# Optimization experiments

Measured on AMD Instinct MI355X. Metric: run time of the kernel, lower is better.

Reference implementation:

```python
import jax, jax.numpy as jnp
import numpy as np

N_NODES, N_GRAPHS, PER_GRAPH, N_EDGES = 20000, 200, 100, 320000
X_DIM, E_DIM, G_DIM = 32, 16, 32
NUM_EMB, HEADS, LAYERS = 64, 2, 3
EPS_GEN, EPS_LN = 1e-7, 1e-5


def _w(k, shape, scale=0.05):
    return (jax.random.normal(k, shape) * scale).astype(jnp.float32)


def _mlp3(x, W1, b1, W2, b2, W3, b3):
    h = jax.nn.leaky_relu(x @ W1 + b1)
    h = jax.nn.leaky_relu(h @ W2 + b2)
    return h @ W3 + b3


def _seg_sum(x, idx, n):
    return jax.ops.segment_sum(x, idx, num_segments=n)


def _seg_mean(x, idx, n):
    s = _seg_sum(x, idx, n)
    cnt = _seg_sum(jnp.ones((x.shape[0],), x.dtype), idx, n)
    return s / jnp.clip(cnt, 1.0, None)[:, None]


def _seg_softmax(logits, idx, n):
    # PyG softmax: subtract per-segment max, normalize with +1e-16
    m = jax.ops.segment_max(logits, idx, num_segments=n)
    m = jnp.where(jnp.isfinite(m), m, 0.0)
    e = jnp.exp(logits - m[idx])
    s = jax.ops.segment_sum(e, idx, num_segments=n)
    return e / (s[idx] + 1e-16)


def _graph_layernorm(x, batch, n_graphs):
    # PyG LayerNorm(mode='graph', affine=False): mean/var over all node-feature
    # entries of each graph.
    f = x.shape[-1]
    cnt = _seg_sum(jnp.ones((x.shape[0],), x.dtype), batch, n_graphs)
    norm = jnp.clip(cnt, 1.0, None) * f
    mean = _seg_sum(x.sum(-1), batch, n_graphs) / norm
    xc = x - mean[batch][:, None]
    var = _seg_sum((xc * xc).sum(-1), batch, n_graphs) / norm
    return xc / jnp.sqrt(var + EPS_LN)[batch][:, None]


def _forward(x, edge_attr, cond, edge_index, batch,
             x2h_W1, x2h_b1, x2h_W2, x2h_b2, x2h_W3, x2h_b3,
             e2h_W1, e2h_b1, e2h_W2, e2h_b2, e2h_W3, e2h_b3,
             c2h_W1, c2h_b1, c2h_W2, c2h_b2, c2h_W3, c2h_b3,
             gen_W, tr_Wq, tr_bq, tr_Wk, tr_bk, tr_Wv, tr_bv, tr_We, tr_Ws, tr_bs,
             lin_W, lin_b, ff_W1, ff_b1, ff_W2, ff_b2):
    N = x.shape[0]
    G = cond.shape[0]
    Naug = N + G
    o = _mlp3(x, x2h_W1, x2h_b1, x2h_W2, x2h_b2, x2h_W3, x2h_b3)
    e = _mlp3(edge_attr, e2h_W1, e2h_b1, e2h_W2, e2h_b2, e2h_W3, e2h_b3)
    c = _mlp3(cond, c2h_W1, c2h_b1, c2h_W2, c2h_b2, c2h_W3, c2h_b3)
    # virtual-node edges: node<->virtual node of its graph (virtual ids = N..N+G-1)
    u = jnp.arange(N, dtype=edge_index.dtype)
    v = batch.astype(edge_index.dtype) + N
    aug_ei = jnp.concatenate([edge_index, jnp.stack([u, v]), jnp.stack([v, u])], axis=1)
    e_p = jnp.zeros((2 * N, NUM_EMB), o.dtype).at[:, 0].set(1.0)
    aug_e = jnp.concatenate([e, e_p], axis=0)
    # add_self_loops(fill_value='mean'): self-loop attr = mean of incoming edge attrs
    loop_attr = _seg_mean(aug_e, aug_ei[1], Naug)
    loops = jnp.arange(Naug, dtype=edge_index.dtype)
    aug_ei = jnp.concatenate([aug_ei, jnp.stack([loops, loops])], axis=1)
    aug_e = jnp.concatenate([aug_e, loop_attr], axis=0)
    aug_batch = jnp.concatenate([batch, jnp.arange(G, dtype=batch.dtype)])
    o = jnp.concatenate([o, c], axis=0)  # [Naug, emb]
    src, dst = aug_ei[0], aug_ei[1]
    scale = 1.0 / float(np.sqrt(NUM_EMB))
    for i in range(LAYERS):
        # GENConv(aggr='add', norm=None, num_layers=1): sum(relu(x_j+e)+eps) + x, then Linear
        msg = jax.nn.relu(o[src] + aug_e) + EPS_GEN
        agg = (_seg_sum(msg, dst, Naug) + o) @ gen_W[i]
        # TransformerConv(2*emb -> emb, heads, edge_dim=emb, concat=True)
        xin = jnp.concatenate([o, agg], axis=1)  # [Naug, 2*emb]
        q = (xin @ tr_Wq[i] + tr_bq[i]).reshape(Naug, HEADS, NUM_EMB)
        k = (xin @ tr_Wk[i] + tr_bk[i]).reshape(Naug, HEADS, NUM_EMB)
        vv = (xin @ tr_Wv[i] + tr_bv[i]).reshape(Naug, HEADS, NUM_EMB)
        eh = (aug_e @ tr_We[i]).reshape(-1, HEADS, NUM_EMB)  # [E, H, C]
        kj = k[src] + eh
        alpha = _seg_softmax(jnp.einsum('ehc,ehc->eh', q[dst], kj) * scale, dst, Naug)
        tout = _seg_sum((vv[src] + eh) * alpha[..., None], dst, Naug)
        tout = tout.reshape(Naug, HEADS * NUM_EMB) + xin @ tr_Ws[i] + tr_bs[i]
        # residual + graph LayerNorm, then FFN + graph LayerNorm
        o = _graph_layernorm(o + tout @ lin_W[i] + lin_b[i], aug_batch, G)
        ff = jax.nn.leaky_relu(o @ ff_W1[i] + ff_b1[i]) @ ff_W2[i] + ff_b2[i]
        o = _graph_layernorm(o + ff, aug_batch, G)
    node_o, virt = o[:N], o[N:]
    glob = jnp.concatenate([_seg_mean(node_o, batch, G), virt, c], axis=1)
    o_final = jnp.concatenate([node_o, c[batch]], axis=1)
    return (o_final, glob)


def setup_inputs() -> dict:
    key = jax.random.key(0)
    ks = iter(jax.random.split(key, 64))
    inp = {}
    inp['x'] = jax.random.normal(next(ks), (N_NODES, X_DIM), dtype=jnp.float32)
    inp['edge_attr'] = jax.random.normal(next(ks), (N_EDGES, E_DIM), dtype=jnp.float32)
    inp['cond'] = jax.random.normal(next(ks), (N_GRAPHS, G_DIM), dtype=jnp.float32)
    src = jax.random.randint(next(ks), (N_EDGES,), 0, N_NODES)
    dst = (src // PER_GRAPH) * PER_GRAPH + jax.random.randint(next(ks), (N_EDGES,), 0, PER_GRAPH)
    inp['edge_index'] = jnp.stack([src, dst]).astype(jnp.int32)
    inp['batch'] = jnp.repeat(jnp.arange(N_GRAPHS, dtype=jnp.int32), PER_GRAPH)
    for p, nin in [('x2h', X_DIM), ('e2h', E_DIM), ('c2h', G_DIM)]:
        inp[p + '_W1'] = _w(next(ks), (nin, NUM_EMB)); inp[p + '_b1'] = _w(next(ks), (NUM_EMB,))
        inp[p + '_W2'] = _w(next(ks), (NUM_EMB, NUM_EMB)); inp[p + '_b2'] = _w(next(ks), (NUM_EMB,))
        inp[p + '_W3'] = _w(next(ks), (NUM_EMB, NUM_EMB)); inp[p + '_b3'] = _w(next(ks), (NUM_EMB,))
    HC = HEADS * NUM_EMB
    inp['gen_W'] = _w(next(ks), (LAYERS, NUM_EMB, NUM_EMB))
    inp['tr_Wq'] = _w(next(ks), (LAYERS, 2 * NUM_EMB, HC)); inp['tr_bq'] = _w(next(ks), (LAYERS, HC))
    inp['tr_Wk'] = _w(next(ks), (LAYERS, 2 * NUM_EMB, HC)); inp['tr_bk'] = _w(next(ks), (LAYERS, HC))
    inp['tr_Wv'] = _w(next(ks), (LAYERS, 2 * NUM_EMB, HC)); inp['tr_bv'] = _w(next(ks), (LAYERS, HC))
    inp['tr_We'] = _w(next(ks), (LAYERS, NUM_EMB, HC))
    inp['tr_Ws'] = _w(next(ks), (LAYERS, 2 * NUM_EMB, HC)); inp['tr_bs'] = _w(next(ks), (LAYERS, HC))
    inp['lin_W'] = _w(next(ks), (LAYERS, HC, NUM_EMB)); inp['lin_b'] = _w(next(ks), (LAYERS, NUM_EMB))
    inp['ff_W1'] = _w(next(ks), (LAYERS, NUM_EMB, 4 * NUM_EMB)); inp['ff_b1'] = _w(next(ks), (LAYERS, 4 * NUM_EMB))
    inp['ff_W2'] = _w(next(ks), (LAYERS, 4 * NUM_EMB, NUM_EMB)); inp['ff_b2'] = _w(next(ks), (LAYERS, NUM_EMB))
    return inp


def reference(x, edge_attr, cond, edge_index, batch,
              x2h_W1, x2h_b1, x2h_W2, x2h_b2, x2h_W3, x2h_b3,
              e2h_W1, e2h_b1, e2h_W2, e2h_b2, e2h_W3, e2h_b3,
              c2h_W1, c2h_b1, c2h_W2, c2h_b2, c2h_W3, c2h_b3,
              gen_W, tr_Wq, tr_bq, tr_Wk, tr_bk, tr_Wv, tr_bv, tr_We, tr_Ws, tr_bs,
              lin_W, lin_b, ff_W1, ff_b1, ff_W2, ff_b2):
    return _forward(x, edge_attr, cond, edge_index, batch,
                    x2h_W1, x2h_b1, x2h_W2, x2h_b2, x2h_W3, x2h_b3,
                    e2h_W1, e2h_b1, e2h_W2, e2h_b2, e2h_W3, e2h_b3,
                    c2h_W1, c2h_b1, c2h_W2, c2h_b2, c2h_W3, c2h_b3,
                    gen_W, tr_Wq, tr_bq, tr_Wk, tr_bk, tr_Wv, tr_bv, tr_We, tr_Ws, tr_bs,
                    lin_W, lin_b, ff_W1, ff_b1, ff_W2, ff_b2)
```

## Files before the change

### kernel.cpp

```cpp
#include <hip/hip_runtime.h>
#include <cstddef>

#define NN   20000
#define NG   200
#define NE   320000
#define NAUG 20200
#define NE2  360000
#define EAUG 380200
#define DD   64
#define HC   128

typedef float  f32x4 __attribute__((ext_vector_type(4)));
typedef short  s16x8 __attribute__((ext_vector_type(8)));

static __device__ __forceinline__ unsigned short bf16r(float f){
  unsigned u = __float_as_uint(f);
  u += 0x7FFFu + ((u >> 16) & 1u);
  return (unsigned short)(u >> 16);
}
static __device__ __forceinline__ float4 b2f4(ushort4 u){
  return make_float4(__uint_as_float((unsigned)u.x << 16),
                     __uint_as_float((unsigned)u.y << 16),
                     __uint_as_float((unsigned)u.z << 16),
                     __uint_as_float((unsigned)u.w << 16));
}
static __device__ __forceinline__ float d4(float4 a, float4 b){
  return a.x*b.x + a.y*b.y + a.z*b.z + a.w*b.w;
}
static __device__ __forceinline__ float4 f4ab(float4 a, float s, float4 b, float t){
  return make_float4(a.x*s + b.x*t, a.y*s + b.y*t, a.z*s + b.z*t, a.w*s + b.w*t);
}
static __device__ __forceinline__ float4 f4s(float4 a, float s){
  return make_float4(a.x*s, a.y*s, a.z*s, a.w*s);
}

#define WTAB_INIT { \
  {0,0,128,128,136,128,0},{0,0,128,128,136,128,16384},{0,0,128,128,136,128,32768}, \
  {1,0,128,128,136,128,0},{1,0,128,128,136,128,16384},{1,0,128,128,136,128,32768}, \
  {2,0,128,128,136,128,0},{2,0,128,128,136,128,16384},{2,0,128,128,136,128,32768}, \
  {3,0,128,128,136,128,0},{3,0,128,128,136,128,16384},{3,0,128,128,136,128,32768}, \
  {4,0,64,64,72,64,0},{4,0,64,64,72,64,4096},{4,0,64,64,72,64,8192}, \
  {5,0,128,64,136,64,0},{5,0,128,64,136,64,8192},{5,0,128,64,136,64,16384}, \
  {6,0,64,256,72,256,0},{6,0,64,256,72,256,16384},{6,0,64,256,72,256,32768}, \
  {7,0,256,64,264,64,0},{7,0,256,64,264,64,16384},{7,0,256,64,264,64,32768}, \
  {8,1,64,64,72,128,0},{8,1,64,64,72,128,64},{8,1,64,64,72,128,8192},{8,1,64,64,72,128,8256},{8,1,64,64,72,128,16384},{8,1,64,64,72,128,16448}, \
  {8,0,64,64,72,128,0},{8,0,64,64,72,128,64},{8,0,64,64,72,128,8192},{8,0,64,64,72,128,8256},{8,0,64,64,72,128,16384},{8,0,64,64,72,128,16448}, \
  {9,0,32,64,40,64,0},{10,0,64,64,72,64,0},{11,0,64,64,72,64,0}, \
  {12,0,16,64,40,64,0},{13,0,64,64,72,64,0},{14,0,64,64,72,64,0}, \
  {15,0,32,64,40,64,0},{16,0,64,64,72,64,0},{17,0,64,64,72,64,0} }

static const int WTAB_H[45][7] = WTAB_INIT;
__device__ static const int WTAB_D[45][7] = WTAB_INIT;

struct WPtrs { const float* p[18]; };

__global__ void wconv_all_k(WPtrs wp, unsigned short* __restrict__ outbase){
  int b = blockIdx.x;
  int acc = 0; unsigned ooff = 0;
  #pragma unroll 1
  for (int j = 0; j < 45; j++){
    int e  = WTAB_D[j][3] * WTAB_D[j][4];
    int nb = (e + 255) >> 8;
    if (b < acc + nb){
      int idx = (b - acc)*256 + threadIdx.x;
      if (idx < e){
        int KP = WTAB_D[j][4];
        int n = idx / KP, k = idx % KP;
        float v = 0.f;
        if (k < WTAB_D[j][2]){
          const float* s = wp.p[WTAB_D[j][0]];
          int st = WTAB_D[j][5], so = WTAB_D[j][6];
          v = (WTAB_D[j][1] == 0) ? s[(size_t)so + (size_t)k*st + n]
                                  : s[(size_t)so + (size_t)n*st + k];
        }
        outbase[ooff + idx] = bf16r(v);
      }
      return;
    }
    acc += nb; ooff += (unsigned)e;
  }
}

template<int NT>
__launch_bounds__(256)
__global__ void gemm_mfma_k(const float* __restrict__ A, const float* __restrict__ A2,
                            int M, int K, int lda,
                            const unsigned short* __restrict__ WtG,
                            const float* __restrict__ bias, int act,
                            const float* __restrict__ res, const float* __restrict__ res2,
                            int rstride, float* __restrict__ out, int ostride){
  extern __shared__ unsigned short smem[];
  const int KC  = (K > 128) ? 128 : K;
  const int KPc = KC + 8;
  const int KP  = K + 8;
  unsigned short* Wts  = smem;
  unsigned short* Asub = smem + NT*KPc;
  const int tid = threadIdx.x;
  const int wid = tid >> 6, lane = tid & 63;
  const int lrow = lane & 15, quad = lane >> 4;
  const int m0 = blockIdx.x * 64;
  f32x4 acc[NT/16];
  #pragma unroll
  for (int t = 0; t < NT/16; t++) acc[t] = (f32x4){0.f,0.f,0.f,0.f};

  for (int k0 = 0; k0 < K; k0 += KC){
    const int wv = NT*KPc/8, wrow = KPc/8;
    for (int i = tid; i < wv; i += 256){
      int n = i / wrow, c8 = i % wrow;
      *(uint4*)&Wts[n*KPc + c8*8] = *(const uint4*)&WtG[(size_t)n*KP + k0 + c8*8];
    }
    const int av = 64*KC/4, arow = KC/4;
    for (int i = tid; i < av; i += 256){
      int r = i / arow, c4i = i % arow;
      int m = m0 + r, k = k0 + c4i*4;
      float4 v = make_float4(0.f,0.f,0.f,0.f);
      if (m < M){
        v = *(const float4*)(A + (size_t)m*lda + k);
        if (A2){ float4 w = *(const float4*)(A2 + (size_t)m*lda + k);
                 v.x += w.x; v.y += w.y; v.z += w.z; v.w += w.w; }
      }
      ushort4 s; s.x = bf16r(v.x); s.y = bf16r(v.y); s.z = bf16r(v.z); s.w = bf16r(v.w);
      *(ushort4*)&Asub[r*KPc + c4i*4] = s;
    }
    __syncthreads();
    const int ksteps = KC >> 5;
    for (int ks = 0; ks < ksteps; ks++){
      s16x8 a = *(const s16x8*)&Asub[(wid*16 + lrow)*KPc + ks*32 + quad*8];
      #pragma unroll
      for (int nt = 0; nt < NT/16; nt++){
        s16x8 b = *(const s16x8*)&Wts[(nt*16 + lrow)*KPc + ks*32 + quad*8];
        acc[nt] = __builtin_amdgcn_mfma_f32_16x16x32_bf16(a, b, acc[nt], 0, 0, 0);
      }
    }
    __syncthreads();
  }

  const int mb = m0 + wid*16 + quad*4;
  #pragma unroll
  for (int nt = 0; nt < NT/16; nt++){
    int n = nt*16 + lrow;
    #pragma unroll
    for (int r = 0; r < 4; r++){
      int m = mb + r;
      if (m < M){
        float v = acc[nt][r];
        if (bias) v += bias[n];
        if (act)  v = v > 0.f ? v : 0.01f*v;
        if (res)  v += res [(size_t)m*rstride + n];
        if (res2) v += res2[(size_t)m*rstride + n];
        out[(size_t)m*ostride + n] = v;
      }
    }
  }
}

struct PW4 { const unsigned short* w[4]; const float* b[4]; };

__launch_bounds__(256)
__global__ void qkvs4_k(const float* __restrict__ A, int M, PW4 pw,
                        float* __restrict__ out){
  __shared__ __align__(16) unsigned short Wts[128*136];
  __shared__ __align__(16) unsigned short Asub[64*136];
  const unsigned short* WtG = pw.w[blockIdx.y];
  const float* bias = pw.b[blockIdx.y];
  const int tid = threadIdx.x;
  const int wid = tid >> 6, lane = tid & 63;
  const int lrow = lane & 15, quad = lane >> 4;
  const int m0 = blockIdx.x * 64;
  for (int i = tid; i < 128*17; i += 256){
    int n = i/17, c8 = i%17;
    *(uint4*)&Wts[n*136 + c8*8] = *(const uint4*)&WtG[(size_t)n*136 + c8*8];
  }
  for (int i = tid; i < 64*32; i += 256){
    int r = i >> 5, c4 = (i & 31)*4;
    int m = m0 + r;
    float4 v = make_float4(0.f,0.f,0.f,0.f);
    if (m < M) v = *(const float4*)(A + (size_t)m*128 + c4);
    ushort4 s; s.x=bf16r(v.x); s.y=bf16r(v.y); s.z=bf16r(v.z); s.w=bf16r(v.w);
    *(ushort4*)&Asub[r*136 + c4] = s;
  }
  __syncthreads();
  f32x4 acc[8];
  #pragma unroll
  for (int t=0;t<8;t++) acc[t] = (f32x4){0.f,0.f,0.f,0.f};
  #pragma unroll
  for (int ks = 0; ks < 4; ks++){
    s16x8 a = *(const s16x8*)&Asub[(wid*16 + lrow)*136 + ks*32 + quad*8];
    #pragma unroll
    for (int nt = 0; nt < 8; nt++){
      s16x8 b = *(const s16x8*)&Wts[(nt*16 + lrow)*136 + ks*32 + quad*8];
      acc[nt] = __builtin_amdgcn_mfma_f32_16x16x32_bf16(a, b, acc[nt], 0, 0, 0);
    }
  }
  const int mb = m0 + wid*16 + quad*4;
  const int yoff = blockIdx.y*128;
  #pragma unroll
  for (int nt = 0; nt < 8; nt++){
    int n = nt*16 + lrow;
    #pragma unroll
    for (int r = 0; r < 4; r++){
      int m = mb + r;
      if (m < M) out[(size_t)m*512 + yoff + n] = acc[nt][r] + bias[n];
    }
  }
}

struct PW2 { const unsigned short* w[2]; };

__launch_bounds__(256)
__global__ void qe2_k(const float* __restrict__ qkvs, int M, PW2 pw,
                      float* __restrict__ qe){
  __shared__ __align__(16) unsigned short Wts[64*72];
  __shared__ __align__(16) unsigned short Asub[64*72];
  const unsigned short* WtG = pw.w[blockIdx.y];
  const int tid = threadIdx.x;
  const int wid = tid >> 6, lane = tid & 63;
  const int lrow = lane & 15, quad = lane >> 4;
  const int m0 = blockIdx.x * 64;
  const int yoff = blockIdx.y * 64;
  for (int i = tid; i < 64*9; i += 256){
    int n = i/9, c8 = i%9;
    *(uint4*)&Wts[n*72 + c8*8] = *(const uint4*)&WtG[(size_t)n*72 + c8*8];
  }
  for (int i = tid; i < 64*16; i += 256){
    int r = i >> 4, c4 = (i & 15)*4;
    int m = m0 + r;
    float4 v = make_float4(0.f,0.f,0.f,0.f);
    if (m < M) v = *(const float4*)(qkvs + (size_t)m*512 + yoff + c4);
    ushort4 s; s.x=bf16r(v.x); s.y=bf16r(v.y); s.z=bf16r(v.z); s.w=bf16r(v.w);
    *(ushort4*)&Asub[r*72 + c4] = s;
  }
  __syncthreads();
  f32x4 acc[4];
  #pragma unroll
  for (int t=0;t<4;t++) acc[t] = (f32x4){0.f,0.f,0.f,0.f};
  #pragma unroll
  for (int ks = 0; ks < 2; ks++){
    s16x8 a = *(const s16x8*)&Asub[(wid*16 + lrow)*72 + ks*32 + quad*8];
    #pragma unroll
    for (int nt = 0; nt < 4; nt++){
      s16x8 b = *(const s16x8*)&Wts[(nt*16 + lrow)*72 + ks*32 + quad*8];
      acc[nt] = __builtin_amdgcn_mfma_f32_16x16x32_bf16(a, b, acc[nt], 0, 0, 0);
    }
  }
  const int mb = m0 + wid*16 + quad*4;
  #pragma unroll
  for (int nt = 0; nt < 4; nt++){
    int n = nt*16 + lrow;
    #pragma unroll
    for (int r = 0; r < 4; r++){
      int m = mb + r;
      if (m < M) qe[(size_t)m*HC + yoff + n] = acc[nt][r];
    }
  }
}

__launch_bounds__(256)
__global__ void tout2_k(const float* __restrict__ wv, int M, PW2 pw,
                        const float* __restrict__ t1, const float* __restrict__ qkvs,
                        float* __restrict__ tout){
  __shared__ __align__(16) unsigned short Wts[64*72];
  __shared__ __align__(16) unsigned short Asub[64*72];
  const unsigned short* WtG = pw.w[blockIdx.y];
  const int tid = threadIdx.x;
  const int wid = tid >> 6, lane = tid & 63;
  const int lrow = lane & 15, quad = lane >> 4;
  const int m0 = blockIdx.x * 64;
  const int yoff = blockIdx.y * 64;
  for (int i = tid; i < 64*9; i += 256){
    int n = i/9, c8 = i%9;
    *(uint4*)&Wts[n*72 + c8*8] = *(const uint4*)&WtG[(size_t)n*72 + c8*8];
  }
  for (int i = tid; i < 64*16; i += 256){
    int r = i >> 4, c4 = (i & 15)*4;
    int m = m0 + r;
    float4 v = make_float4(0.f,0.f,0.f,0.f);
    if (m < M) v = *(const float4*)(wv + (size_t)m*HC + yoff + c4);
    ushort4 s; s.x=bf16r(v.x); s.y=bf16r(v.y); s.z=bf16r(v.z); s.w=bf16r(v.w);
    *(ushort4*)&Asub[r*72 + c4] = s;
  }
  __syncthreads();
  f32x4 acc[4];
  #pragma unroll
  for (int t=0;t<4;t++) acc[t] = (f32x4){0.f,0.f,0.f,0.f};
  #pragma unroll
  for (int ks = 0; ks < 2; ks++){
    s16x8 a = *(const s16x8*)&Asub[(wid*16 + lrow)*72 + ks*32 + quad*8];
    #pragma unroll
    for (int nt = 0; nt < 4; nt++){
      s16x8 b = *(const s16x8*)&Wts[(nt*16 + lrow)*72 + ks*32 + quad*8];
      acc[nt] = __builtin_amdgcn_mfma_f32_16x16x32_bf16(a, b, acc[nt], 0, 0, 0);
    }
  }
  const int mb = m0 + wid*16 + quad*4;
  #pragma unroll
  for (int nt = 0; nt < 4; nt++){
    int n = nt*16 + lrow;
    #pragma unroll
    for (int r = 0; r < 4; r++){
      int m = mb + r;
      if (m < M)
        tout[(size_t)m*HC + yoff + n] = acc[nt][r]
          + t1[(size_t)m*HC + yoff + n] + qkvs[(size_t)m*512 + 384 + yoff + n];
    }
  }
}

__launch_bounds__(256)
__global__ void mlp3_mfma_k(const float* __restrict__ X, int M, int Din,
                            const unsigned short* __restrict__ w1t,
                            const unsigned short* __restrict__ w2t,
                            const unsigned short* __restrict__ w3t,
                            const float* __restrict__ b1, const float* __restrict__ b2,
                            const float* __restrict__ b3, float* __restrict__ out){
  __shared__ __align__(16) unsigned short W1s[64*40], W2s[64*72], W3s[64*72];
  __shared__ __align__(16) unsigned short xs[64*40], hs[64*72];
  __shared__ float bsh[192];
  const int tid = threadIdx.x;
  for (int i = tid; i < 320; i += 256)  *(uint4*)&W1s[i*8] = *(const uint4*)&w1t[i*8];
  for (int i = tid; i < 576; i += 256){ *(uint4*)&W2s[i*8] = *(const uint4*)&w2t[i*8];
                                        *(uint4*)&W3s[i*8] = *(const uint4*)&w3t[i*8]; }
  if (tid < 64){ bsh[tid] = b1[tid]; bsh[64+tid] = b2[tid]; bsh[128+tid] = b3[tid]; }
  const int m0 = blockIdx.x * 64;
  for (int i = tid; i < 512; i += 256){
    int r = i >> 3, c4 = (i & 7) * 4;
    int m = m0 + r;
    float4 v = make_float4(0.f,0.f,0.f,0.f);
    if (m < M && c4 < Din) v = *(const float4*)(X + (size_t)m*Din + c4);
    ushort4 s; s.x = bf16r(v.x); s.y = bf16r(v.y); s.z = bf16r(v.z); s.w = bf16r(v.w);
    *(ushort4*)&xs[r*40 + c4] = s;
  }
  __syncthreads();
  const int wid = tid >> 6, lane = tid & 63;
  const int lrow = lane & 15, quad = lane >> 4;
  f32x4 acc[4];

  #pragma unroll
  for (int t = 0; t < 4; t++) acc[t] = (f32x4){0.f,0.f,0.f,0.f};
  {
    s16x8 a = *(const s16x8*)&xs[(wid*16 + lrow)*40 + quad*8];
    #pragma unroll
    for (int nt = 0; nt < 4; nt++){
      s16x8 b = *(const s16x8*)&W1s[(nt*16 + lrow)*40 + quad*8];
      acc[nt] = __builtin_amdgcn_mfma_f32_16x16x32_bf16(a, b, acc[nt], 0, 0, 0);
    }
  }
  #pragma unroll
  for (int nt = 0; nt < 4; nt++){
    int n = nt*16 + lrow;
    #pragma unroll
    for (int r = 0; r < 4; r++){
      float v = acc[nt][r] + bsh[n];
      v = v > 0.f ? v : 0.01f*v;
      hs[(wid*16 + quad*4 + r)*72 + n] = bf16r(v);
    }
  }
  __syncthreads();

  #pragma unroll
  for (int t = 0; t < 4; t++) acc[t] = (f32x4){0.f,0.f,0.f,0.f};
  #pragma unroll
  for (int ks = 0; ks < 2; ks++){
    s16x8 a = *(const s16x8*)&hs[(wid*16 + lrow)*72 + ks*32 + quad*8];
    #pragma unroll
    for (int nt = 0; nt < 4; nt++){
      s16x8 b = *(const s16x8*)&W2s[(nt*16 + lrow)*72 + ks*32 + quad*8];
      acc[nt] = __builtin_amdgcn_mfma_f32_16x16x32_bf16(a, b, acc[nt], 0, 0, 0);
    }
  }
  __syncthreads();
  #pragma unroll
  for (int nt = 0; nt < 4; nt++){
    int n = nt*16 + lrow;
    #pragma unroll
    for (int r = 0; r < 4; r++){
      float v = acc[nt][r] + bsh[64 + n];
      v = v > 0.f ? v : 0.01f*v;
      hs[(wid*16 + quad*4 + r)*72 + n] = bf16r(v);
    }
  }
  __syncthreads();

  #pragma unroll
  for (int t = 0; t < 4; t++) acc[t] = (f32x4){0.f,0.f,0.f,0.f};
  #pragma unroll
  for (int ks = 0; ks < 2; ks++){
    s16x8 a = *(const s16x8*)&hs[(wid*16 + lrow)*72 + ks*32 + quad*8];
    #pragma unroll
    for (int nt = 0; nt < 4; nt++){
      s16x8 b = *(const s16x8*)&W3s[(nt*16 + lrow)*72 + ks*32 + quad*8];
      acc[nt] = __builtin_amdgcn_mfma_f32_16x16x32_bf16(a, b, acc[nt], 0, 0, 0);
    }
  }
  #pragma unroll
  for (int nt = 0; nt < 4; nt++){
    int n = nt*16 + lrow;
    #pragma unroll
    for (int r = 0; r < 4; r++){
      int m = m0 + wid*16 + quad*4 + r;
      if (m < M) out[(size_t)m*64 + n] = acc[nt][r] + bsh[128 + n];
    }
  }
}

__global__ void build_edges_k(const int* __restrict__ ei, const int* __restrict__ batch,
                              int* __restrict__ srcA, int* __restrict__ dstA){
  int idx = blockIdx.x*256 + threadIdx.x;
  if (idx >= EAUG) return;
  int s, d;
  if (idx < NE)          { s = ei[idx];              d = ei[NE+idx]; }
  else if (idx < NE+NN)  { int i = idx-NE;           s = i;            d = batch[i]+NN; }
  else if (idx < NE2)    { int i = idx-(NE+NN);      s = batch[i]+NN;  d = i; }
  else                   { int i = idx-NE2;          s = i;            d = i; }
  srcA[idx]=s; dstA[idx]=d;
}

__global__ void count_k(const int* __restrict__ dstA, int* __restrict__ cnt){
  int e = blockIdx.x*256 + threadIdx.x;
  if (e < EAUG) atomicAdd(&cnt[dstA[e]], 1);
}

__global__ void scan_k(const int* __restrict__ cnt, int* __restrict__ rowptr){
  __shared__ int part[1024];
  int tid = threadIdx.x;
  const int per = (NAUG + 1023) / 1024;
  int base = tid * per;
  int s = 0;
  for (int i=0;i<per;i++){ int idx=base+i; if (idx<NAUG) s += cnt[idx]; }
  part[tid] = s;
  __syncthreads();
  for (int off=1; off<1024; off<<=1){
    int v = (tid>=off) ? part[tid-off] : 0;
    __syncthreads();
    part[tid] += v;
    __syncthreads();
  }
  int run = (tid==0) ? 0 : part[tid-1];
  for (int i=0;i<per;i++){
    int idx=base+i;
    if (idx<NAUG){ rowptr[idx]=run; run += cnt[idx]; }
  }
  if (tid==0) rowptr[NAUG] = EAUG;
}

__global__ void scatter_k(const int* __restrict__ srcA, const int* __restrict__ dstA,
                          const int* __restrict__ rowptr, int* __restrict__ cursor,
                          int* __restrict__ eid, int* __restrict__ esrc){
  int e = blockIdx.x*256 + threadIdx.x;
  if (e >= EAUG) return;
  int d = dstA[e];
  int pos = rowptr[d] + atomicAdd(&cursor[d], 1);
  eid[pos]  = e;
  esrc[pos] = srcA[e];
}

__global__ void set_ep_k(float* __restrict__ aug_e){
  int idx = blockIdx.x*256 + threadIdx.x;
  if (idx >= 2*NN*DD) return;
  int c = idx & 63;
  aug_e[(size_t)NE*DD + idx] = (c==0) ? 1.f : 0.f;
}

__launch_bounds__(256)
__global__ void loopmean_k(const int* __restrict__ rowptr, const int* __restrict__ eid,
                           float* __restrict__ aug_e){
  int tid = threadIdx.x;
  int d = blockIdx.x*16 + (tid>>4);
  if (d >= NAUG) return;
  int t4 = (tid & 15)*4;
  int beg = rowptr[d], end = rowptr[d+1];
  float4 s = make_float4(0.f,0.f,0.f,0.f); int n = 0;
  for (int p=beg; p<end; p++){
    int e = eid[p];
    if (e < NE2){
      float4 a = *(const float4*)(aug_e + (size_t)e*DD + t4);
      s.x += a.x; s.y += a.y; s.z += a.z; s.w += a.w;
      n++;
    }
  }
  float cv = (n < 1) ? 1.f : (float)n;
  *(float4*)(aug_e + (size_t)(NE2+d)*DD + t4) = f4s(s, 1.f/cv);
}

__launch_bounds__(512)
__global__ void msg_graph_k(const float* __restrict__ o, const float* __restrict__ aug_e,
                            const int* __restrict__ rowptr, const int* __restrict__ eid,
                            const int* __restrict__ esrc, float* __restrict__ aggsum){
  __shared__ __align__(16) float OS[101*72];
  const int g = blockIdx.x;
  const int tid = threadIdx.x;
  for (int i = tid; i < 101*16; i += 512){
    int ln = i >> 4, c4 = (i & 15)*4;
    int row = (ln < 100) ? g*100 + ln : NN + g;
    *(float4*)&OS[ln*72 + c4] = *(const float4*)(o + (size_t)row*DD + c4);
  }
  __syncthreads();
  const int gr = tid >> 4;
  const int t4 = (tid & 15)*4;
  for (int ld = gr; ld < 101; ld += 32){
    int d = (ld < 100) ? g*100 + ld : NN + g;
    int beg = rowptr[d], end = rowptr[d+1];
    float4 acc = make_float4(0.f,0.f,0.f,0.f);
    for (int p=beg; p<end; p++){
      int e = eid[p], s = esrc[p];
      int ls = (s >= NN) ? 100 : (s - g*100);
      float4 ov = *(const float4*)&OS[ls*72 + t4];
      float4 ae = *(const float4*)(aug_e + (size_t)e*DD + t4);
      acc.x += fmaxf(ov.x+ae.x, 0.f) + 1e-7f;
      acc.y += fmaxf(ov.y+ae.y, 0.f) + 1e-7f;
      acc.z += fmaxf(ov.z+ae.z, 0.f) + 1e-7f;
      acc.w += fmaxf(ov.w+ae.w, 0.f) + 1e-7f;
    }
    *(float4*)(aggsum + (size_t)d*DD + t4) = acc;
  }
}

__global__ void copy_o_xin_k(const float* __restrict__ o, float* __restrict__ xin){
  int idx = blockIdx.x*256 + threadIdx.x;
  if (idx >= NAUG*DD) return;
  int n = idx >> 6, c = idx & 63;
  xin[(size_t)n*HC + c] = o[idx];
}

__launch_bounds__(512)
__global__ void attn_graph_k(const float* __restrict__ qkvs, const float* __restrict__ qe,
                             const float* __restrict__ aug_e,
                             const int* __restrict__ rowptr, const int* __restrict__ eid,
                             const int* __restrict__ esrc,
                             float* __restrict__ t1, float* __restrict__ wbuf){
  __shared__ __align__(16) unsigned short KV[101*264];
  const int g = blockIdx.x;
  const int tid = threadIdx.x;
  for (int i = tid; i < 101*64; i += 512){
    int ln = i >> 6, c4 = (i & 63)*4;
    int row = (ln < 100) ? g*100 + ln : NN + g;
    float4 v = *(const float4*)(qkvs + (size_t)row*512 + 128 + c4);
    ushort4 s; s.x=bf16r(v.x); s.y=bf16r(v.y); s.z=bf16r(v.z); s.w=bf16r(v.w);
    *(ushort4*)&KV[ln*264 + c4] = s;
  }
  __syncthreads();
  const int gr = tid >> 4;
  const int t4 = (tid & 15)*4;
  for (int ld = gr; ld < 101; ld += 32){
    int d = (ld < 100) ? g*100 + ld : NN + g;
    const float* qr = qkvs + (size_t)d*512;
    float4 q0  = *(const float4*)(qr + t4);
    float4 q1  = *(const float4*)(qr + 64 + t4);
    float4 qe0 = *(const float4*)(qe + (size_t)d*HC + t4);
    float4 qe1 = *(const float4*)(qe + (size_t)d*HC + 64 + t4);
    float m0=-1e30f, m1=-1e30f, l0=0.f, l1=0.f;
    float4 a0 = make_float4(0.f,0.f,0.f,0.f), a1 = a0, w0 = a0, w1 = a0;
    int beg = rowptr[d], end = rowptr[d+1];
    for (int p=beg; p<end; p++){
      int e = eid[p], s = esrc[p];
      int ls = (s >= NN) ? 100 : (s - g*100);
      const unsigned short* kr = &KV[ls*264];
      float4 k0 = b2f4(*(const ushort4*)(kr + t4));
      float4 k1 = b2f4(*(const ushort4*)(kr + 64 + t4));
      float4 v0 = b2f4(*(const ushort4*)(kr + 128 + t4));
      float4 v1 = b2f4(*(const ushort4*)(kr + 192 + t4));
      float4 ae = *(const float4*)(aug_e + (size_t)e*DD + t4);
      float p0 = d4(q0,k0) + d4(qe0,ae);
      float p1 = d4(q1,k1) + d4(qe1,ae);
      p0 += __shfl_xor(p0,8); p0 += __shfl_xor(p0,4); p0 += __shfl_xor(p0,2); p0 += __shfl_xor(p0,1);
      p1 += __shfl_xor(p1,8); p1 += __shfl_xor(p1,4); p1 += __shfl_xor(p1,2); p1 += __shfl_xor(p1,1);
      p0 *= 0.125f; p1 *= 0.125f;
      float nm0 = fmaxf(m0, p0);
      float sc0 = __expf(m0 - nm0);
      float e0  = __expf(p0 - nm0);
      l0 = l0*sc0 + e0; a0 = f4ab(a0, sc0, v0, e0); w0 = f4ab(w0, sc0, ae, e0); m0 = nm0;
      float nm1 = fmaxf(m1, p1);
      float sc1 = __expf(m1 - nm1);
      float e1  = __expf(p1 - nm1);
      l1 = l1*sc1 + e1; a1 = f4ab(a1, sc1, v1, e1); w1 = f4ab(w1, sc1, ae, e1); m1 = nm1;
    }
    float i0 = 1.f/(l0 + 1e-16f), i1 = 1.f/(l1 + 1e-16f);
    *(float4*)(t1   + (size_t)d*HC + t4)      = f4s(a0, i0);
    *(float4*)(t1   + (size_t)d*HC + 64 + t4) = f4s(a1, i1);
    *(float4*)(wbuf + (size_t)d*HC + t4)      = f4s(w0, i0);
    *(float4*)(wbuf + (size_t)d*HC + 64 + t4) = f4s(w1, i1);
  }
}

__global__ void ln_k(const float* __restrict__ y, float* __restrict__ o){
  int g = blockIdx.x, tid = threadIdx.x;
  float sum=0.f, ss=0.f;
  for (int i=tid; i<101*64; i+=256){
    int nd=i>>6, c=i&63;
    int row = (nd<100) ? g*100+nd : NN+g;
    float v = y[(size_t)row*DD + c];
    sum += v; ss += v*v;
  }
  #pragma unroll
  for (int off=32; off; off>>=1){ sum += __shfl_xor(sum, off); ss += __shfl_xor(ss, off); }
  __shared__ float s1[4], s2[4];
  if ((tid&63)==0){ s1[tid>>6]=sum; s2[tid>>6]=ss; }
  __syncthreads();
  sum = s1[0]+s1[1]+s1[2]+s1[3];
  ss  = s2[0]+s2[1]+s2[2]+s2[3];
  const float inv = 1.f/6464.f;
  float mean = sum*inv;
  float var  = ss*inv - mean*mean;
  float rstd = rsqrtf(var + 1e-5f);
  for (int i=tid; i<101*64; i+=256){
    int nd=i>>6, c=i&63;
    int row = (nd<100) ? g*100+nd : NN+g;
    o[(size_t)row*DD + c] = (y[(size_t)row*DD + c] - mean)*rstd;
  }
}

__global__ void copy_c_o_k(const float* __restrict__ c_emb, float* __restrict__ o){
  int idx = blockIdx.x*256 + threadIdx.x;
  if (idx >= NG*DD) return;
  o[(size_t)NN*DD + idx] = c_emb[idx];
}

__global__ void glob_k(const float* __restrict__ o, const float* __restrict__ c_emb,
                       float* __restrict__ gout){
  int g = blockIdx.x, c = threadIdx.x;
  float acc = 0.f;
  for (int t=0;t<100;t++) acc += o[(size_t)(g*100+t)*DD + c];
  gout[(size_t)g*192 + c]       = acc / 100.f;
  gout[(size_t)g*192 + 64 + c]  = o[(size_t)(NN+g)*DD + c];
  gout[(size_t)g*192 + 128 + c] = c_emb[(size_t)g*DD + c];
}
__global__ void ofinal_k(const float* __restrict__ o, const float* __restrict__ c_emb,
                         const int* __restrict__ batch, float* __restrict__ out){
  int idx = blockIdx.x*256 + threadIdx.x;
  if (idx >= NN*HC) return;
  int n = idx>>7, j = idx&127;
  out[idx] = (j<64) ? o[(size_t)n*DD + j] : c_emb[(size_t)batch[n]*DD + (j-64)];
}

static inline int cdiv(int a, int b){ return (a+b-1)/b; }

static inline void gemm_mfma(int N, const float* A, const float* A2, int M, int K, int lda,
                             const unsigned short* Wt, const float* bias, int act,
                             const float* res, const float* res2, int rstride,
                             float* out, int ostride, hipStream_t st){
  int KC = (K > 128) ? 128 : K;
  int KPc = KC + 8;
  size_t sh = (size_t)(N*KPc + 64*KPc) * 2;
  int grid = cdiv(M, 64);
  if (N == 64)
    gemm_mfma_k<64><<<grid,256,sh,st>>>(A,A2,M,K,lda,Wt,bias,act,res,res2,rstride,out,ostride);
  else if (N == 128)
    gemm_mfma_k<128><<<grid,256,sh,st>>>(A,A2,M,K,lda,Wt,bias,act,res,res2,rstride,out,ostride);
  else
    gemm_mfma_k<256><<<grid,256,sh,st>>>(A,A2,M,K,lda,Wt,bias,act,res,res2,rstride,out,ostride);
}

extern "C" void kernel_launch(void* const* d_in, const int* in_sizes, int n_in,
                              void* d_out, int out_size, void* d_ws, size_t ws_size,
                              hipStream_t stream){
  (void)in_sizes; (void)n_in; (void)out_size;
  const float* x         = (const float*)d_in[0];
  const float* edge_attr = (const float*)d_in[1];
  const float* cond      = (const float*)d_in[2];
  const int*   edge_index= (const int*)  d_in[3];
  const int*   batch     = (const int*)  d_in[4];
  const float* xW1=(const float*)d_in[5],  *xb1=(const float*)d_in[6],
             * xW2=(const float*)d_in[7],  *xb2=(const float*)d_in[8],
             * xW3=(const float*)d_in[9],  *xb3=(const float*)d_in[10];
  const float* eW1=(const float*)d_in[11], *eb1=(const float*)d_in[12],
             * eW2=(const float*)d_in[13], *eb2=(const float*)d_in[14],
             * eW3=(const float*)d_in[15], *eb3=(const float*)d_in[16];
  const float* cW1=(const float*)d_in[17], *cb1=(const float*)d_in[18],
             * cW2=(const float*)d_in[19], *cb2=(const float*)d_in[20],
             * cW3=(const float*)d_in[21], *cb3=(const float*)d_in[22];
  const float* gen_W=(const float*)d_in[23];
  const float* trWq=(const float*)d_in[24], *trbq=(const float*)d_in[25];
  const float* trWk=(const float*)d_in[26], *trbk=(const float*)d_in[27];
  const float* trWv=(const float*)d_in[28], *trbv=(const float*)d_in[29];
  const float* trWe=(const float*)d_in[30];
  const float* trWs=(const float*)d_in[31], *trbs=(const float*)d_in[32];
  const float* linW=(const float*)d_in[33], *linb=(const float*)d_in[34];
  const float* ffW1=(const float*)d_in[35], *ffb1=(const float*)d_in[36];
  const float* ffW2=(const float*)d_in[37], *ffb2=(const float*)d_in[38];
  float* out = (float*)d_out;

  float* ws = (float*)d_ws;
  size_t off = 0;
  auto alloc = [&](size_t n)->float*{ float* p = ws + off; off += (n + 63) & ~(size_t)63; return p; };
  int*      srcA  = (int*)alloc(EAUG);
  int*      dstA  = (int*)alloc(EAUG);
  int*      cnt   = (int*)alloc(NAUG);
  int*      rowptr= (int*)alloc(NAUG+1);
  int*      cursor= (int*)alloc(NAUG);
  int*      eid   = (int*)alloc(EAUG);
  int*      esrc  = (int*)alloc(EAUG);
  float*    aug_e = alloc((size_t)EAUG*DD);
  float*    o     = alloc((size_t)NAUG*DD);
  float*    c_emb = alloc((size_t)NG*DD);
  float*    ybuf  = alloc((size_t)NAUG*DD);
  float*    aggsum= alloc((size_t)NAUG*DD);
  float*    xin   = alloc((size_t)NAUG*HC);
  float*    xqkvs = alloc((size_t)NAUG*512);
  float*    qeb   = alloc((size_t)NAUG*HC);
  float*    toutb = alloc((size_t)NAUG*HC);
  float*    t1    = alloc((size_t)NAUG*HC);
  float*    wbuf  = alloc((size_t)NAUG*HC);
  float*    ffh   = alloc((size_t)NAUG*256);
  unsigned short* warena = (unsigned short*)alloc(222720);
  if (off*sizeof(float) > ws_size) return;

  const unsigned short* wptr[45];
  int wblk = 0;
  { size_t woff = 0;
    for (int j = 0; j < 45; j++){
      wptr[j] = warena + woff;
      int e = WTAB_H[j][3]*WTAB_H[j][4];
      woff += (size_t)e;
      wblk += cdiv(e, 256);
    } }

  WPtrs wp;
  wp.p[0]=trWq; wp.p[1]=trWk; wp.p[2]=trWv; wp.p[3]=trWs; wp.p[4]=gen_W;
  wp.p[5]=linW; wp.p[6]=ffW1; wp.p[7]=ffW2; wp.p[8]=trWe;
  wp.p[9]=xW1; wp.p[10]=xW2; wp.p[11]=xW3;
  wp.p[12]=eW1; wp.p[13]=eW2; wp.p[14]=eW3;
  wp.p[15]=cW1; wp.p[16]=cW2; wp.p[17]=cW3;
  wconv_all_k<<<wblk,256,0,stream>>>(wp, warena);

  build_edges_k<<<cdiv(EAUG,256),256,0,stream>>>(edge_index, batch, srcA, dstA);
  hipMemsetAsync(cnt, 0, sizeof(int)*NAUG, stream);
  hipMemsetAsync(cursor, 0, sizeof(int)*NAUG, stream);
  count_k<<<cdiv(EAUG,256),256,0,stream>>>(dstA, cnt);
  scan_k<<<1,1024,0,stream>>>(cnt, rowptr);
  scatter_k<<<cdiv(EAUG,256),256,0,stream>>>(srcA, dstA, rowptr, cursor, eid, esrc);

  mlp3_mfma_k<<<cdiv(NN,64),256,0,stream>>>(x,        NN, 32, wptr[36],wptr[37],wptr[38], xb1,xb2,xb3, o);
  mlp3_mfma_k<<<cdiv(NG,64),256,0,stream>>>(cond,     NG, 32, wptr[42],wptr[43],wptr[44], cb1,cb2,cb3, c_emb);
  mlp3_mfma_k<<<cdiv(NE,64),256,0,stream>>>(edge_attr,NE, 16, wptr[39],wptr[40],wptr[41], eb1,eb2,eb3, aug_e);
  set_ep_k<<<cdiv(2*NN*DD,256),256,0,stream>>>(aug_e);
  loopmean_k<<<cdiv(NAUG,16),256,0,stream>>>(rowptr, eid, aug_e);
  copy_c_o_k<<<cdiv(NG*DD,256),256,0,stream>>>(c_emb, o);

  for (int L=0; L<3; L++){
    const float* lb_i = linb + (size_t)L*DD;
    const float* f1b  = ffb1 + (size_t)L*256;
    const float* f2b  = ffb2 + (size_t)L*DD;
    const unsigned short* genT = wptr[12+L], *linT = wptr[15+L], *ff1T = wptr[18+L], *ff2T = wptr[21+L];
    PW4 pw4; pw4.w[0]=wptr[0+L]; pw4.w[1]=wptr[3+L]; pw4.w[2]=wptr[6+L]; pw4.w[3]=wptr[9+L];
    pw4.b[0]=trbq+(size_t)L*HC; pw4.b[1]=trbk+(size_t)L*HC;
    pw4.b[2]=trbv+(size_t)L*HC; pw4.b[3]=trbs+(size_t)L*HC;
    PW2 pwE; pwE.w[0]=wptr[24+2*L]; pwE.w[1]=wptr[25+2*L];
    PW2 pwT; pwT.w[0]=wptr[30+2*L]; pwT.w[1]=wptr[31+2*L];

    msg_graph_k<<<NG,512,0,stream>>>(o, aug_e, rowptr, eid, esrc, aggsum);
    copy_o_xin_k<<<cdiv(NAUG*DD,256),256,0,stream>>>(o, xin);
    gemm_mfma( 64, aggsum, o, NAUG, 64, 64, genT, nullptr, 0, nullptr, nullptr, 0, xin+64, HC, stream);
    qkvs4_k<<<dim3(cdiv(NAUG,64),4),256,0,stream>>>(xin, NAUG, pw4, xqkvs);
    qe2_k<<<dim3(cdiv(NAUG,64),2),256,0,stream>>>(xqkvs, NAUG, pwE, qeb);
    attn_graph_k<<<NG,512,0,stream>>>(xqkvs, qeb, aug_e, rowptr, eid, esrc, t1, wbuf);
    tout2_k<<<dim3(cdiv(NAUG,64),2),256,0,stream>>>(wbuf, NAUG, pwT, t1, xqkvs, toutb);
    gemm_mfma( 64, toutb, nullptr, NAUG, 128, 128, linT, lb_i, 0, o, nullptr, DD, ybuf, DD, stream);
    ln_k<<<NG,256,0,stream>>>(ybuf, o);
    gemm_mfma(256, o,   nullptr, NAUG,  64,  64, ff1T, f1b, 1, nullptr, nullptr, 0, ffh, 256, stream);
    gemm_mfma( 64, ffh, nullptr, NAUG, 256, 256, ff2T, f2b, 0, o, nullptr, DD, ybuf, DD, stream);
    ln_k<<<NG,256,0,stream>>>(ybuf, o);
  }

  glob_k<<<NG,64,0,stream>>>(o, c_emb, out + (size_t)NN*HC);
  ofinal_k<<<cdiv(NN*HC,256),256,0,stream>>>(o, c_emb, batch, out);
}
```

Before: 1.466 ms.

## Store edge embeddings in CSR order and split per-graph kernels across two blocks

Edge features are now written directly in destination-sorted CSR order using a per-edge position map, so the message and attention kernels read them contiguously by CSR position instead of gathering through eid. Per-graph source indices are preloaded into shared memory as bytes. The msg and attn kernels launch two blocks per graph, each handling half of the destination nodes, to raise occupancy. In exchange the edge MLP and init kernels now do scattered writes, and the node embeddings are loaded into shared memory twice per graph.

```diff
diff --git a/kernel.cpp b/kernel.cpp
--- a/kernel.cpp
+++ b/kernel.cpp
@@ -312,7 +312,8 @@
                             const unsigned short* __restrict__ w2t,
                             const unsigned short* __restrict__ w3t,
                             const float* __restrict__ b1, const float* __restrict__ b2,
-                            const float* __restrict__ b3, float* __restrict__ out){
+                            const float* __restrict__ b3,
+                            const int* __restrict__ perm, float* __restrict__ out){
   __shared__ __align__(16) unsigned short W1s[64*40], W2s[64*72], W3s[64*72];
   __shared__ __align__(16) unsigned short xs[64*40], hs[64*72];
   __shared__ float bsh[192];
@@ -398,7 +399,10 @@
     #pragma unroll
     for (int r = 0; r < 4; r++){
       int m = m0 + wid*16 + quad*4 + r;
-      if (m < M) out[(size_t)m*64 + n] = acc[nt][r] + bsh[128 + n];
+      if (m < M){
+        int orow = perm ? perm[m] : m;
+        out[(size_t)orow*64 + n] = acc[nt][r] + bsh[128 + n];
+      }
     }
   }
 }
@@ -445,25 +449,27 @@
 
 __global__ void scatter_k(const int* __restrict__ srcA, const int* __restrict__ dstA,
                           const int* __restrict__ rowptr, int* __restrict__ cursor,
-                          int* __restrict__ eid, int* __restrict__ esrc){
+                          int* __restrict__ eid, int* __restrict__ esrc,
+                          int* __restrict__ epos){
   int e = blockIdx.x*256 + threadIdx.x;
   if (e >= EAUG) return;
   int d = dstA[e];
   int pos = rowptr[d] + atomicAdd(&cursor[d], 1);
   eid[pos]  = e;
   esrc[pos] = srcA[e];
-}
-
-__global__ void set_ep_k(float* __restrict__ aug_e){
+  epos[e]   = pos;
+}
+
+__global__ void set_ep_k(const int* __restrict__ epos, float* __restrict__ aug_p){
   int idx = blockIdx.x*256 + threadIdx.x;
   if (idx >= 2*NN*DD) return;
-  int c = idx & 63;
-  aug_e[(size_t)NE*DD + idx] = (c==0) ? 1.f : 0.f;
+  int i = idx >> 6, c = idx & 63;
+  aug_p[(size_t)epos[NE + i]*DD + c] = (c==0) ? 1.f : 0.f;
 }
 
 __launch_bounds__(256)
 __global__ void loopmean_k(const int* __restrict__ rowptr, const int* __restrict__ eid,
-                           float* __restrict__ aug_e){
+                           const int* __restrict__ epos, float* __restrict__ aug_p){
   int tid = threadIdx.x;
   int d = blockIdx.x*16 + (tid>>4);
   if (d >= NAUG) return;
@@ -473,39 +479,57 @@
   for (int p=beg; p<end; p++){
     int e = eid[p];
     if (e < NE2){
-      float4 a = *(const float4*)(aug_e + (size_t)e*DD + t4);
+      float4 a = *(const float4*)(aug_p + (size_t)p*DD + t4);
       s.x += a.x; s.y += a.y; s.z += a.z; s.w += a.w;
       n++;
     }
   }
   float cv = (n < 1) ? 1.f : (float)n;
-  *(float4*)(aug_e + (size_t)(NE2+d)*DD + t4) = f4s(s, 1.f/cv);
+  *(float4*)(aug_p + (size_t)epos[NE2+d]*DD + t4) = f4s(s, 1.f/cv);
 }
 
 __launch_bounds__(512)
-__global__ void msg_graph_k(const float* __restrict__ o, const float* __restrict__ aug_e,
-                            const int* __restrict__ rowptr, const int* __restrict__ eid,
+__global__ void msg_graph_k(const float* __restrict__ o, const float* __restrict__ aug_p,
+                            const int* __restrict__ rowptr,
                             const int* __restrict__ esrc, float* __restrict__ aggsum){
   __shared__ __align__(16) float OS[101*72];
-  const int g = blockIdx.x;
+  __shared__ unsigned char EL[3072];
+  const int g = blockIdx.x >> 1, half = blockIdx.x & 1;
   const int tid = threadIdx.x;
   for (int i = tid; i < 101*16; i += 512){
     int ln = i >> 4, c4 = (i & 15)*4;
     int row = (ln < 100) ? g*100 + ln : NN + g;
     *(float4*)&OS[ln*72 + c4] = *(const float4*)(o + (size_t)row*DD + c4);
   }
-  __syncthreads();
-  const int gr = tid >> 4;
-  const int t4 = (tid & 15)*4;
-  for (int ld = gr; ld < 101; ld += 32){
-    int d = (ld < 100) ? g*100 + ld : NN + g;
-    int beg = rowptr[d], end = rowptr[d+1];
+  const int baseA = rowptr[g*100];
+  const int lenA  = rowptr[g*100 + 100] - baseA;
+  const int baseB = rowptr[NN + g];
+  const int lenB  = rowptr[NN + g + 1] - baseB;
+  const bool useL = (lenA + lenB) <= 3072;
+  if (useL){
+    for (int i = tid; i < lenA; i += 512){
+      int s = esrc[baseA + i];
+      EL[i] = (unsigned char)((s >= NN) ? 100 : (s - g*100));
+    }
+    for (int i = tid; i < lenB; i += 512){
+      int s = esrc[baseB + i];
+      EL[lenA + i] = (unsigned char)((s >= NN) ? 100 : (s - g*100));
+    }
+  }
+  __syncthreads();
+  const int gr = tid >> 4, t4 = (tid & 15)*4;
+  const int ld0 = half ? 51 : 0, ld1 = half ? 101 : 51;
+  for (int ld = ld0 + gr; ld < ld1; ld += 32){
+    int d, pbeg, pend, eofs;
+    if (ld < 100){ d = g*100 + ld; pbeg = rowptr[d]; pend = rowptr[d+1]; eofs = -baseA; }
+    else         { d = NN + g;     pbeg = baseB;     pend = baseB + lenB; eofs = lenA - baseB; }
     float4 acc = make_float4(0.f,0.f,0.f,0.f);
-    for (int p=beg; p<end; p++){
-      int e = eid[p], s = esrc[p];
-      int ls = (s >= NN) ? 100 : (s - g*100);
+    for (int p = pbeg; p < pend; p++){
+      int ls;
+      if (useL) ls = EL[p + eofs];
+      else { int s = esrc[p]; ls = (s >= NN) ? 100 : (s - g*100); }
       float4 ov = *(const float4*)&OS[ls*72 + t4];
-      float4 ae = *(const float4*)(aug_e + (size_t)e*DD + t4);
+      float4 ae = *(const float4*)(aug_p + (size_t)p*DD + t4);
       acc.x += fmaxf(ov.x+ae.x, 0.f) + 1e-7f;
       acc.y += fmaxf(ov.y+ae.y, 0.f) + 1e-7f;
       acc.z += fmaxf(ov.z+ae.z, 0.f) + 1e-7f;
@@ -524,12 +548,13 @@
 
 __launch_bounds__(512)
 __global__ void attn_graph_k(const float* __restrict__ qkvs, const float* __restrict__ qe,
-                             const float* __restrict__ aug_e,
-                             const int* __restrict__ rowptr, const int* __restrict__ eid,
+                             const float* __restrict__ aug_p,
+                             const int* __restrict__ rowptr,
                              const int* __restrict__ esrc,
                              float* __restrict__ t1, float* __restrict__ wbuf){
   __shared__ __align__(16) unsigned short KV[101*264];
-  const int g = blockIdx.x;
+  __shared__ unsigned char EL[3072];
+  const int g = blockIdx.x >> 1, half = blockIdx.x & 1;
   const int tid = threadIdx.x;
   for (int i = tid; i < 101*64; i += 512){
     int ln = i >> 6, c4 = (i & 63)*4;
@@ -538,11 +563,28 @@
     ushort4 s; s.x=bf16r(v.x); s.y=bf16r(v.y); s.z=bf16r(v.z); s.w=bf16r(v.w);
     *(ushort4*)&KV[ln*264 + c4] = s;
   }
-  __syncthreads();
-  const int gr = tid >> 4;
-  const int t4 = (tid & 15)*4;
-  for (int ld = gr; ld < 101; ld += 32){
-    int d = (ld < 100) ? g*100 + ld : NN + g;
+  const int baseA = rowptr[g*100];
+  const int lenA  = rowptr[g*100 + 100] - baseA;
+  const int baseB = rowptr[NN + g];
+  const int lenB  = rowptr[NN + g + 1] - baseB;
+  const bool useL = (lenA + lenB) <= 3072;
+  if (useL){
+    for (int i = tid; i < lenA; i += 512){
+      int s = esrc[baseA + i];
+      EL[i] = (unsigned char)((s >= NN) ? 100 : (s - g*100));
+    }
+    for (int i = tid; i < lenB; i += 512){
+      int s = esrc[baseB + i];
+      EL[lenA + i] = (unsigned char)((s >= NN) ? 100 : (s - g*100));
+    }
+  }
+  __syncthreads();
+  const int gr = tid >> 4, t4 = (tid & 15)*4;
+  const int ld0 = half ? 51 : 0, ld1 = half ? 101 : 51;
+  for (int ld = ld0 + gr; ld < ld1; ld += 32){
+    int d, pbeg, pend, eofs;
+    if (ld < 100){ d = g*100 + ld; pbeg = rowptr[d]; pend = rowptr[d+1]; eofs = -baseA; }
+    else         { d = NN + g;     pbeg = baseB;     pend = baseB + lenB; eofs = lenA - baseB; }
     const float* qr = qkvs + (size_t)d*512;
     float4 q0  = *(const float4*)(qr + t4);
     float4 q1  = *(const float4*)(qr + 64 + t4);
@@ -550,16 +592,16 @@
     float4 qe1 = *(const float4*)(qe + (size_t)d*HC + 64 + t4);
     float m0=-1e30f, m1=-1e30f, l0=0.f, l1=0.f;
     float4 a0 = make_float4(0.f,0.f,0.f,0.f), a1 = a0, w0 = a0, w1 = a0;
-    int beg = rowptr[d], end = rowptr[d+1];
-    for (int p=beg; p<end; p++){
-      int e = eid[p], s = esrc[p];
-      int ls = (s >= NN) ? 100 : (s - g*100);
+    for (int p = pbeg; p < pend; p++){
+      int ls;
+      if (useL) ls = EL[p + eofs];
+      else { int s = esrc[p]; ls = (s >= NN) ? 100 : (s - g*100); }
       const unsigned short* kr = &KV[ls*264];
       float4 k0 = b2f4(*(const ushort4*)(kr + t4));
       float4 k1 = b2f4(*(const ushort4*)(kr + 64 + t4));
       float4 v0 = b2f4(*(const ushort4*)(kr + 128 + t4));
       float4 v1 = b2f4(*(const ushort4*)(kr + 192 + t4));
-      float4 ae = *(const float4*)(aug_e + (size_t)e*DD + t4);
+      float4 ae = *(const float4*)(aug_p + (size_t)p*DD + t4);
       float p0 = d4(q0,k0) + d4(qe0,ae);
       float p1 = d4(q1,k1) + d4(qe1,ae);
       p0 += __shfl_xor(p0,8); p0 += __shfl_xor(p0,4); p0 += __shfl_xor(p0,2); p0 += __shfl_xor(p0,1);
@@ -689,7 +731,8 @@
   int*      cursor= (int*)alloc(NAUG);
   int*      eid   = (int*)alloc(EAUG);
   int*      esrc  = (int*)alloc(EAUG);
-  float*    aug_e = alloc((size_t)EAUG*DD);
+  int*      epos  = (int*)alloc(EAUG);
+  float*    aug_p = alloc((size_t)EAUG*DD);
   float*    o     = alloc((size_t)NAUG*DD);
   float*    c_emb = alloc((size_t)NG*DD);
   float*    ybuf  = alloc((size_t)NAUG*DD);
@@ -727,13 +770,13 @@
   hipMemsetAsync(cursor, 0, sizeof(int)*NAUG, stream);
   count_k<<<cdiv(EAUG,256),256,0,stream>>>(dstA, cnt);
   scan_k<<<1,1024,0,stream>>>(cnt, rowptr);
-  scatter_k<<<cdiv(EAUG,256),256,0,stream>>>(srcA, dstA, rowptr, cursor, eid, esrc);
-
-  mlp3_mfma_k<<<cdiv(NN,64),256,0,stream>>>(x,        NN, 32, wptr[36],wptr[37],wptr[38], xb1,xb2,xb3, o);
-  mlp3_mfma_k<<<cdiv(NG,64),256,0,stream>>>(cond,     NG, 32, wptr[42],wptr[43],wptr[44], cb1,cb2,cb3, c_emb);
-  mlp3_mfma_k<<<cdiv(NE,64),256,0,stream>>>(edge_attr,NE, 16, wptr[39],wptr[40],wptr[41], eb1,eb2,eb3, aug_e);
-  set_ep_k<<<cdiv(2*NN*DD,256),256,0,stream>>>(aug_e);
-  loopmean_k<<<cdiv(NAUG,16),256,0,stream>>>(rowptr, eid, aug_e);
+  scatter_k<<<cdiv(EAUG,256),256,0,stream>>>(srcA, dstA, rowptr, cursor, eid, esrc, epos);
+
+  mlp3_mfma_k<<<cdiv(NN,64),256,0,stream>>>(x,        NN, 32, wptr[36],wptr[37],wptr[38], xb1,xb2,xb3, nullptr, o);
+  mlp3_mfma_k<<<cdiv(NG,64),256,0,stream>>>(cond,     NG, 32, wptr[42],wptr[43],wptr[44], cb1,cb2,cb3, nullptr, c_emb);
+  mlp3_mfma_k<<<cdiv(NE,64),256,0,stream>>>(edge_attr,NE, 16, wptr[39],wptr[40],wptr[41], eb1,eb2,eb3, epos, aug_p);
+  set_ep_k<<<cdiv(2*NN*DD,256),256,0,stream>>>(epos, aug_p);
+  loopmean_k<<<cdiv(NAUG,16),256,0,stream>>>(rowptr, eid, epos, aug_p);
   copy_c_o_k<<<cdiv(NG*DD,256),256,0,stream>>>(c_emb, o);
 
   for (int L=0; L<3; L++){
@@ -747,12 +790,12 @@
     PW2 pwE; pwE.w[0]=wptr[24+2*L]; pwE.w[1]=wptr[25+2*L];
     PW2 pwT; pwT.w[0]=wptr[30+2*L]; pwT.w[1]=wptr[31+2*L];
 
-    msg_graph_k<<<NG,512,0,stream>>>(o, aug_e, rowptr, eid, esrc, aggsum);
+    msg_graph_k<<<2*NG,512,0,stream>>>(o, aug_p, rowptr, esrc, aggsum);
     copy_o_xin_k<<<cdiv(NAUG*DD,256),256,0,stream>>>(o, xin);
     gemm_mfma( 64, aggsum, o, NAUG, 64, 64, genT, nullptr, 0, nullptr, nullptr, 0, xin+64, HC, stream);
     qkvs4_k<<<dim3(cdiv(NAUG,64),4),256,0,stream>>>(xin, NAUG, pw4, xqkvs);
     qe2_k<<<dim3(cdiv(NAUG,64),2),256,0,stream>>>(xqkvs, NAUG, pwE, qeb);
-    attn_graph_k<<<NG,512,0,stream>>>(xqkvs, qeb, aug_e, rowptr, eid, esrc, t1, wbuf);
+    attn_graph_k<<<2*NG,512,0,stream>>>(xqkvs, qeb, aug_p, rowptr, esrc, t1, wbuf);
     tout2_k<<<dim3(cdiv(NAUG,64),2),256,0,stream>>>(wbuf, NAUG, pwT, t1, xqkvs, toutb);
     gemm_mfma( 64, toutb, nullptr, NAUG, 128, 128, linT, lb_i, 0, o, nullptr, DD, ybuf, DD, stream);
     ln_k<<<NG,256,0,stream>>>(ybuf, o);
```

New measurement: 1.289 ms. -12.1%, faster.
